# Optimization experiments

Measured on AMD Instinct MI355X. Metric: run time of the kernel, lower is better.

Reference implementation:

```python
import jax, jax.numpy as jnp
import numpy as np

N_DIS = 25000   # disease nodes: indices [0, 25000)
N_MIR = 25000   # mirna nodes:  indices [25000, 50000)
N = N_DIS + N_MIR
E = 600000
EMB = 128
HID = 128


def setup_inputs() -> dict:
    key = jax.random.key(0)
    ks = jax.random.split(key, 14)
    d_features = jax.random.normal(ks[0], (N_DIS, 383), jnp.float32)
    m_features = jax.random.normal(ks[1], (N_MIR, 495), jnp.float32)
    src = jax.random.randint(ks[2], (E,), 0, N, jnp.int32)
    dst = jax.random.randint(ks[3], (E,), 0, N, jnp.int32)
    def lin(k, fan_in, fan_out):
        lim = 1.0 / np.sqrt(fan_in)
        return jax.random.uniform(k, (fan_in, fan_out), jnp.float32, -lim, lim)
    return {
        "d_features": d_features,
        "m_features": m_features,
        "src": src,
        "dst": dst,
        "W_d": lin(ks[4], 383, EMB), "b_d": jnp.zeros((EMB,), jnp.float32),
        "W_m": lin(ks[5], 495, EMB), "b_m": jnp.zeros((EMB,), jnp.float32),
        "W_self1": lin(ks[6], EMB, HID), "W_neigh1": lin(ks[7], EMB, HID),
        "b1": jnp.zeros((HID,), jnp.float32),
        "W_self2": lin(ks[8], HID, HID), "W_neigh2": lin(ks[9], HID, HID),
        "b2": jnp.zeros((HID,), jnp.float32),
    }


def reference(d_features, m_features, src, dst,
              W_d, b_d, W_m, b_m,
              W_self1, W_neigh1, b1, W_self2, W_neigh2, b2):
    # Per-type embedding projection (torch.no_grad in original; dropout eval=identity)
    h_d = d_features @ W_d + b_d            # [N_DIS, EMB]
    h_m = m_features @ W_m + b_m            # [N_MIR, EMB]
    h = jnp.concatenate([h_d, h_m], axis=0)  # [N, EMB]

    # in-degree for mean aggregation (isolated nodes -> mean 0, like DGL fn.mean)
    deg = jax.ops.segment_sum(jnp.ones(src.shape, h.dtype), dst, num_segments=N)
    inv_deg = 1.0 / jnp.maximum(deg, 1.0)    # [N]

    def sage(x, W_self, W_neigh, b):
        # gather src feats, segment-mean into dst, then combine (DGL SAGEConv 'mean')
        agg = jax.ops.segment_sum(x[src], dst, num_segments=N) * inv_deg[:, None]
        return x @ W_self + agg @ W_neigh + b

    h = jax.nn.relu(sage(h, W_self1, W_neigh1, b1))
    h = sage(h, W_self2, W_neigh2, b2)
    return h
```

## Files before the change

### kernel.cpp

```cpp
#include <hip/hip_runtime.h>

#define N_DIS 25000
#define N_MIR 25000
#define NN    50000
#define E_NUM 600000
#define EMB   128

typedef __attribute__((ext_vector_type(8))) short short8v;
typedef __attribute__((ext_vector_type(4))) float floatx4;

__device__ __forceinline__ floatx4 mfma_bf16_16x16x32(short8v a, short8v b, floatx4 c) {
    asm("v_mfma_f32_16x16x32_bf16 %0, %1, %2, %0" : "+v"(c) : "v"(a), "v"(b));
    return c;
}

__device__ __forceinline__ float us2f(unsigned short u) {
    return __uint_as_float(((unsigned)u) << 16);
}
__device__ __forceinline__ unsigned short f2us(float f) {
    unsigned u = __float_as_uint(f);
    unsigned r = ((u >> 16) & 1u) + 0x7FFFu;
    u += r;
    return (unsigned short)(u >> 16);
}
__device__ __forceinline__ float loadf(const void* p, size_t i, bool isbf) {
    if (isbf) return us2f(((const unsigned short*)p)[i]);
    return ((const float*)p)[i];
}

__global__ __launch_bounds__(256) void gs_zero(int* counts, int* flags) {
    int i = blockIdx.x * blockDim.x + threadIdx.x;
    if (i < NN) counts[i] = 0;
    if (i < 8) flags[i] = 0;
}

__global__ __launch_bounds__(64) void gs_setflag(int* flags, int v) {
    if (threadIdx.x == 0) flags[0] = v;
}

__global__ __launch_bounds__(256) void gs_probe(const void* x, int* flags) {
    const unsigned* u = (const unsigned*)x;
    unsigned w = u[threadIdx.x];
    int e = (int)((w >> 7) & 0xFF);
    if (e >= 118 && e <= 135) atomicAdd(&flags[0], 1);
}

__global__ __launch_bounds__(256) void gs_prepw(const void* Wd, const void* Wm,
                                                const void* Ws1, const void* Wn1,
                                                const void* Ws2, const void* Wn2,
                                                const int* flags, unsigned short* wt) {
    const bool isbf = flags[0] > 128;
    const int t = threadIdx.x;
    const int w = blockIdx.x >> 2;
    const int cq = (blockIdx.x & 3) * 32;
    const void* W;
    unsigned short* oh;
    unsigned short* ol;
    int K, Kp;
    if (w == 0)      { W = Wd;  oh = wt + 0;      ol = wt + 49152;  K = 383; Kp = 384; }
    else if (w == 1) { W = Wm;  oh = wt + 98304;  ol = wt + 163840; K = 495; Kp = 512; }
    else if (w == 2) { W = Ws1; oh = wt + 229376; ol = wt + 245760; K = 128; Kp = 128; }
    else if (w == 3) { W = Wn1; oh = wt + 262144; ol = wt + 278528; K = 128; Kp = 128; }
    else if (w == 4) { W = Ws2; oh = wt + 294912; ol = wt + 311296; K = 128; Kp = 128; }
    else             { W = Wn2; oh = wt + 327680; ol = wt + 344064; K = 128; Kp = 128; }
    for (int c = cq; c < cq + 32; ++c) {
        for (int k = t; k < Kp; k += 256) {
            float x = (k < K) ? loadf(W, (size_t)k * EMB + c, isbf) : 0.f;
            unsigned short h = f2us(x);
            oh[(size_t)c * Kp + k] = h;
            ol[(size_t)c * Kp + k] = f2us(x - us2f(h));
        }
    }
}

__global__ __launch_bounds__(256) void gs_count(const int* dst, int* counts) {
    int e = blockIdx.x * blockDim.x + threadIdx.x;
    if (e < E_NUM) {
        unsigned d = (unsigned)dst[e];
        if (d < (unsigned)NN) atomicAdd(&counts[d], 1);
    }
}

__global__ __launch_bounds__(256) void gs_scan1(const int* counts, int* row_start, int* bsums) {
    __shared__ int tsum[256];
    const int t = threadIdx.x;
    const int base = blockIdx.x * 1024 + t * 4;
    int v0 = (base + 0 < NN) ? counts[base + 0] : 0;
    int v1 = (base + 1 < NN) ? counts[base + 1] : 0;
    int v2 = (base + 2 < NN) ? counts[base + 2] : 0;
    int v3 = (base + 3 < NN) ? counts[base + 3] : 0;
    int s = v0 + v1 + v2 + v3;
    tsum[t] = s;
    __syncthreads();
    for (int off = 1; off < 256; off <<= 1) {
        int xv = 0;
        if (t >= off) xv = tsum[t - off];
        __syncthreads();
        tsum[t] += xv;
        __syncthreads();
    }
    int excl = tsum[t] - s;
    if (base + 0 < NN) row_start[base + 0] = excl;
    excl += v0;
    if (base + 1 < NN) row_start[base + 1] = excl;
    excl += v1;
    if (base + 2 < NN) row_start[base + 2] = excl;
    excl += v2;
    if (base + 3 < NN) row_start[base + 3] = excl;
    if (t == 255) bsums[blockIdx.x] = tsum[255];
}

__global__ __launch_bounds__(64) void gs_scan2(int* bsums, int* row_start, int nb) {
    if (threadIdx.x == 0) {
        int run = 0;
        for (int i = 0; i < nb; ++i) {
            int v = bsums[i];
            bsums[i] = run;
            run += v;
        }
        row_start[NN] = run;
    }
}

__global__ __launch_bounds__(256) void gs_scan3(int* row_start, int* cursor, const int* bsums) {
    const int t = threadIdx.x;
    const int base = blockIdx.x * 1024 + t * 4;
    const int add = bsums[blockIdx.x];
    for (int i = 0; i < 4; ++i) {
        int idx = base + i;
        if (idx < NN) {
            int v = row_start[idx] + add;
            row_start[idx] = v;
            cursor[idx] = v;
        }
    }
}

__global__ __launch_bounds__(256) void gs_scatter(const int* src, const int* dst, int* cursor,
                                                  int* eidx) {
    int e = blockIdx.x * blockDim.x + threadIdx.x;
    if (e < E_NUM) {
        unsigned d = (unsigned)dst[e];
        unsigned sv = (unsigned)src[e];
        if (d < (unsigned)NN && sv < (unsigned)NN) {
            int p = atomicAdd(&cursor[d], 1);
            eidx[p] = (int)sv;
        }
    }
}

__global__ __launch_bounds__(256) void gs_agg(const float* __restrict__ x,
                                              const int* __restrict__ row_start,
                                              const int* __restrict__ eidx,
                                              float* __restrict__ agg) {
    const int t = threadIdx.x;
    const int row = blockIdx.x * 8 + (t >> 5);
    const int tc = (t & 31) * 4;
    if (row >= NN) return;
    const int s0 = row_start[row];
    const int s1 = row_start[row + 1];
    float a0x = 0.f, a0y = 0.f, a0z = 0.f, a0w = 0.f;
    float a1x = 0.f, a1y = 0.f, a1z = 0.f, a1w = 0.f;
    int e = s0;
    for (; e + 1 < s1; e += 2) {
        int sa = eidx[e];
        int sb = eidx[e + 1];
        float4 va = *(const float4*)&x[(size_t)sa * EMB + tc];
        float4 vb = *(const float4*)&x[(size_t)sb * EMB + tc];
        a0x += va.x; a0y += va.y; a0z += va.z; a0w += va.w;
        a1x += vb.x; a1y += vb.y; a1z += vb.z; a1w += vb.w;
    }
    if (e < s1) {
        int sa = eidx[e];
        float4 va = *(const float4*)&x[(size_t)sa * EMB + tc];
        a0x += va.x; a0y += va.y; a0z += va.z; a0w += va.w;
    }
    float inv = (s1 > s0) ? 1.f / (float)(s1 - s0) : 0.f;
    float4 o;
    o.x = (a0x + a1x) * inv;
    o.y = (a0y + a1y) * inv;
    o.z = (a0z + a1z) * inv;
    o.w = (a0w + a1w) * inv;
    *(float4*)&agg[(size_t)row * EMB + tc] = o;
}

__global__ __launch_bounds__(256, 3) void gs_mm(
    const void* __restrict__ Xa, int Ka, const unsigned short* __restrict__ WAh,
    const unsigned short* __restrict__ WAl, int KpA, const void* __restrict__ ba,
    const void* __restrict__ Xb, int Kb, const unsigned short* __restrict__ WBh,
    const unsigned short* __restrict__ WBl, int KpB, const void* __restrict__ bb,
    int splitB, int Ma, int Mb,
    const float* __restrict__ X2, const unsigned short* __restrict__ W2h,
    const unsigned short* __restrict__ W2l,
    const int* __restrict__ flags, float* __restrict__ out, int x1_dyn, int do_relu) {
    __shared__ __align__(16) unsigned char sm[49152];
    unsigned char* smXH = sm;
    unsigned char* smXL = sm + 8192;
    unsigned char* smWH = sm + 16384;
    unsigned char* smWL = sm + 32768;
    const bool isbf = flags[0] > 128;
    const int t = threadIdx.x;
    const bool sideB = (int)blockIdx.x >= splitB;
    const void* X1 = sideB ? Xb : Xa;
    const unsigned short* W1h = sideB ? WBh : WAh;
    const unsigned short* W1l = sideB ? WBl : WAl;
    const int K1 = sideB ? Kb : Ka;
    const int Kp1 = sideB ? KpB : KpA;
    const void* bias = sideB ? bb : ba;
    const int M = sideB ? Mb : Ma;
    const int r0 = (sideB ? ((int)blockIdx.x - splitB) : (int)blockIdx.x) * 64;
    float* outb = out + (sideB ? (size_t)Ma * EMB : 0);
    const bool x1bf = (x1_dyn != 0) && isbf;

    const int l = t & 63;
    const int wv = t >> 6;
    const int wr = wv >> 1, wc = wv & 1;
    const int lr = l & 15, lg = l >> 4;

    floatx4 acc[2][4];
#pragma unroll
    for (int rt = 0; rt < 2; ++rt)
#pragma unroll
        for (int ct = 0; ct < 4; ++ct) acc[rt][ct] = (floatx4){0.f, 0.f, 0.f, 0.f};

    const int nch1 = (K1 + 63) >> 6;
    const int totch = nch1 + (X2 ? 2 : 0);

    const int srX = t >> 2;
    const int skX = (t & 3) << 4;
    const int scW = t >> 1;
    const int skW = (t & 1) << 5;

    for (int ch = 0; ch < totch; ++ch) {
        const void* cX;
        const unsigned short* cWh;
        const unsigned short* cWl;
        int ck0, cK, cKp;
        bool cxbf;
        if (ch < nch1) {
            cX = X1; cWh = W1h; cWl = W1l; ck0 = ch << 6; cK = K1; cKp = Kp1; cxbf = x1bf;
        } else {
            cX = (const void*)X2; cWh = W2h; cWl = W2l;
            ck0 = (ch - nch1) << 6; cK = 128; cKp = 128; cxbf = false;
        }

        __syncthreads();
        {
            const int gr = r0 + srX;
            float xv[16];
            const bool vec = (!cxbf) && (cK == 128);
            if (vec) {
                if (gr < M) {
                    const float* p = &((const float*)cX)[(size_t)gr * 128 + ck0 + skX];
#pragma unroll
                    for (int q = 0; q < 4; ++q) {
                        float4 v = *(const float4*)(p + (q << 2));
                        xv[q * 4 + 0] = v.x; xv[q * 4 + 1] = v.y;
                        xv[q * 4 + 2] = v.z; xv[q * 4 + 3] = v.w;
                    }
                } else {
#pragma unroll
                    for (int j = 0; j < 16; ++j) xv[j] = 0.f;
                }
            } else {
#pragma unroll
                for (int j = 0; j < 16; ++j) {
                    int gk = ck0 + skX + j;
                    float v = 0.f;
                    if (gr < M && gk < cK)
                        v = cxbf ? us2f(((const unsigned short*)cX)[(size_t)gr * cK + gk])
                                 : ((const float*)cX)[(size_t)gr * cK + gk];
                    xv[j] = v;
                }
            }
            const int rowoff = srX << 7;
            const int swz = (srX & 7) << 4;
#pragma unroll
            for (int g = 0; g < 2; ++g) {
                short8v vh, vl;
#pragma unroll
                for (int e = 0; e < 8; ++e) {
                    float x = xv[(g << 3) + e];
                    unsigned short h = f2us(x);
                    vh[e] = (short)h;
                    vl[e] = (short)f2us(x - us2f(h));
                }
                const int off = rowoff + ((((skX << 1) + (g << 4))) ^ swz);
                *(short8v*)(smXH + off) = vh;
                *(short8v*)(smXL + off) = vl;
            }
        }
        {
            const unsigned short* ph = cWh + (size_t)scW * cKp + ck0 + skW;
            const unsigned short* pl = cWl + (size_t)scW * cKp + ck0 + skW;
            const int coff = scW << 7;
            const int csw = (scW & 7) << 4;
#pragma unroll
            for (int g = 0; g < 4; ++g) {
                short8v vh = *(const short8v*)(ph + (g << 3));
                short8v vl = *(const short8v*)(pl + (g << 3));
                const int off = coff + ((((skW << 1) + (g << 4))) ^ csw);
                *(short8v*)(smWH + off) = vh;
                *(short8v*)(smWL + off) = vl;
            }
        }
        __syncthreads();

        const bool skip_xl = cxbf;
        const bool skip_wl = isbf;
#pragma unroll
        for (int ks = 0; ks < 2; ++ks) {
            const int kbyte = (ks << 6) + (lg << 4);
            short8v ah[2], al[2];
#pragma unroll
            for (int rt = 0; rt < 2; ++rt) {
                const int row = wr * 32 + rt * 16 + lr;
                const int off = (row << 7) + (kbyte ^ ((row & 7) << 4));
                ah[rt] = *(const short8v*)(smXH + off);
                al[rt] = *(const short8v*)(smXL + off);
            }
#pragma unroll
            for (int ct = 0; ct < 4; ++ct) {
                const int col = wc * 64 + ct * 16 + lr;
                const int boff = (col << 7) + (kbyte ^ ((col & 7) << 4));
                short8v bh = *(const short8v*)(smWH + boff);
                short8v bl = *(const short8v*)(smWL + boff);
                acc[0][ct] = mfma_bf16_16x16x32(ah[0], bh, acc[0][ct]);
                acc[1][ct] = mfma_bf16_16x16x32(ah[1], bh, acc[1][ct]);
                if (!skip_xl) {
                    acc[0][ct] = mfma_bf16_16x16x32(al[0], bh, acc[0][ct]);
                    acc[1][ct] = mfma_bf16_16x16x32(al[1], bh, acc[1][ct]);
                }
                if (!skip_wl) {
                    acc[0][ct] = mfma_bf16_16x16x32(ah[0], bl, acc[0][ct]);
                    acc[1][ct] = mfma_bf16_16x16x32(ah[1], bl, acc[1][ct]);
                }
            }
        }
    }

#pragma unroll
    for (int ct = 0; ct < 4; ++ct) {
        const int col = wc * 64 + ct * 16 + lr;
        const float bbv = loadf(bias, col, isbf);
#pragma unroll
        for (int rt = 0; rt < 2; ++rt) {
#pragma unroll
            for (int rr = 0; rr < 4; ++rr) {
                const int row = r0 + wr * 32 + rt * 16 + (lg << 2) + rr;
                if (row < M) {
                    float v = acc[rt][ct][rr] + bbv;
                    if (do_relu) v = v > 0.f ? v : 0.f;
                    outb[(size_t)row * EMB + col] = v;
                }
            }
        }
    }
}

extern "C" __attribute__((visibility("default"))) void kernel_launch(
    void* const* d_in, const int* in_sizes, int n_in, void* d_out, int out_size, void* d_ws,
    size_t ws_size, hipStream_t stream) {
    int iDF = 0, iMF = 1, iSRC = 2, iDST = 3, iWD = 4, iBD = 5, iWM = 6, iBM = 7;
    int iWS1 = 8, iWN1 = 9, iB1 = 10, iWS2 = 11, iWN2 = 12, iB2 = 13;
    long u0 = in_sizes ? (long)in_sizes[0] : 9575000L;
    int dt = -1;
    if (u0 == 49024L || u0 == 98048L || u0 == 196096L) {
        iWD = 0; iWM = 1; iWN1 = 2; iWN2 = 3; iWS1 = 4; iWS2 = 5;
        iB1 = 6; iB2 = 7; iBD = 8; iBM = 9; iDF = 10; iDST = 11; iMF = 12; iSRC = 13;
        if (u0 == 98048L) dt = 1;
        else if (u0 == 196096L) dt = 0;
    } else {
        if (u0 == 19150000L) dt = 1;
        else if (u0 == 38300000L) dt = 0;
    }
    const void* d_features = d_in[iDF];
    const void* m_features = d_in[iMF];
    const int* src = (const int*)d_in[iSRC];
    const int* dst = (const int*)d_in[iDST];
    const void* W_d = d_in[iWD];
    const void* b_d = d_in[iBD];
    const void* W_m = d_in[iWM];
    const void* b_m = d_in[iBM];
    const void* W_self1 = d_in[iWS1];
    const void* W_neigh1 = d_in[iWN1];
    const void* b1 = d_in[iB1];
    const void* W_self2 = d_in[iWS2];
    const void* W_neigh2 = d_in[iWN2];
    const void* b2v = d_in[iB2];

    char* w = (char*)d_ws;
    int* flags = (int*)(w + 0);
    int* counts = (int*)(w + 64);
    int* row_start = (int*)(w + 200064);
    int* cursor = (int*)(w + 400128);
    int* bsums = (int*)(w + 600128);
    int* eidx = (int*)(w + 600384);
    unsigned short* wt = (unsigned short*)(w + 3000448);
    unsigned short* wt_hd = wt + 0;
    unsigned short* wt_ld = wt + 49152;
    unsigned short* wt_hm = wt + 98304;
    unsigned short* wt_lm = wt + 163840;
    unsigned short* wt_hs1 = wt + 229376;
    unsigned short* wt_ls1 = wt + 245760;
    unsigned short* wt_hn1 = wt + 262144;
    unsigned short* wt_ln1 = wt + 278528;
    unsigned short* wt_hs2 = wt + 294912;
    unsigned short* wt_ls2 = wt + 311296;
    unsigned short* wt_hn2 = wt + 327680;
    unsigned short* wt_ln2 = wt + 344064;
    float* hF = (float*)(w + 3721344);
    float* h1F = (float*)(w + 29321344);

    const int NB_SCAN = (NN + 1023) / 1024;
    const int EB = (E_NUM + 255) / 256;
    const int ZB = (NN + 255) / 256;

    hipLaunchKernelGGL(gs_zero, dim3(ZB), dim3(256), 0, stream, counts, flags);
    if (dt == 1)
        hipLaunchKernelGGL(gs_setflag, dim3(1), dim3(64), 0, stream, flags, 1000);
    else if (dt == 0)
        hipLaunchKernelGGL(gs_setflag, dim3(1), dim3(64), 0, stream, flags, 0);
    else
        hipLaunchKernelGGL(gs_probe, dim3(1), dim3(256), 0, stream, d_features, flags);

    hipLaunchKernelGGL(gs_prepw, dim3(24), dim3(256), 0, stream, W_d, W_m, W_self1, W_neigh1,
                       W_self2, W_neigh2, flags, wt);

    hipLaunchKernelGGL(gs_count, dim3(EB), dim3(256), 0, stream, dst, counts);
    hipLaunchKernelGGL(gs_scan1, dim3(NB_SCAN), dim3(256), 0, stream, counts, row_start, bsums);
    hipLaunchKernelGGL(gs_scan2, dim3(1), dim3(64), 0, stream, bsums, row_start, NB_SCAN);
    hipLaunchKernelGGL(gs_scan3, dim3(NB_SCAN), dim3(256), 0, stream, row_start, cursor, bsums);
    hipLaunchKernelGGL(gs_scatter, dim3(EB), dim3(256), 0, stream, src, dst, cursor, eidx);

    const int PBd = (N_DIS + 63) / 64;
    hipLaunchKernelGGL(gs_mm, dim3(2 * PBd), dim3(256), 0, stream,
                       d_features, 383, wt_hd, wt_ld, 384, b_d,
                       m_features, 495, wt_hm, wt_lm, 512, b_m,
                       PBd, N_DIS, N_MIR,
                       (const float*)nullptr, (const unsigned short*)nullptr,
                       (const unsigned short*)nullptr,
                       flags, hF, 1, 0);

    const int AB = NN / 8;
    const int GB = (NN + 63) / 64;

    hipLaunchKernelGGL(gs_agg, dim3(AB), dim3(256), 0, stream, hF, row_start, eidx,
                       (float*)d_out);
    hipLaunchKernelGGL(gs_mm, dim3(GB), dim3(256), 0, stream,
                       (const void*)hF, 128, wt_hs1, wt_ls1, 128, b1,
                       (const void*)nullptr, 0, (const unsigned short*)nullptr,
                       (const unsigned short*)nullptr, 0, (const void*)nullptr,
                       GB, NN, 0,
                       (const float*)d_out, wt_hn1, wt_ln1,
                       flags, h1F, 0, 1);

    hipLaunchKernelGGL(gs_agg, dim3(AB), dim3(256), 0, stream, h1F, row_start, eidx, hF);
    hipLaunchKernelGGL(gs_mm, dim3(GB), dim3(256), 0, stream,
                       (const void*)h1F, 128, wt_hs2, wt_ls2, 128, b2v,
                       (const void*)nullptr, 0, (const unsigned short*)nullptr,
                       (const unsigned short*)nullptr, 0, (const void*)nullptr,
                       GB, NN, 0,
                       (const float*)hF, wt_hn2, wt_ln2,
                       flags, (float*)d_out, 0, 0);
}
```

Before: 462.1 us.

## Prefetch next K-chunk into registers while MFMAs consume current LDS tile

Splits the GEMM main loop into descriptor, global-fetch and LDS-write steps. The global loads for chunk ch+1 are now issued into registers before the MFMA work on chunk ch, so load latency can overlap compute. Low-part loads and stores of X and W are skipped when the inputs are already bf16. The hi split now truncates instead of rounding, with the residual carrying the difference. This adds register pressure from the 16-word X buffer plus 8 short8v W buffers, which may reduce occupancy.

```diff
diff --git a/kernel.cpp b/kernel.cpp
--- a/kernel.cpp
+++ b/kernel.cpp
@@ -231,82 +231,108 @@
     const int scW = t >> 1;
     const int skW = (t & 1) << 5;
 
-    for (int ch = 0; ch < totch; ++ch) {
-        const void* cX;
-        const unsigned short* cWh;
-        const unsigned short* cWl;
-        int ck0, cK, cKp;
-        bool cxbf;
+    unsigned xr[16];
+    short8v wfh[4], wfl[4];
+
+    const void* cX;
+    const unsigned short* cWh;
+    const unsigned short* cWl;
+    int ck0, cK, cKp;
+    bool cxbf, cvec;
+    auto DESC = [&](int ch) {
         if (ch < nch1) {
             cX = X1; cWh = W1h; cWl = W1l; ck0 = ch << 6; cK = K1; cKp = Kp1; cxbf = x1bf;
         } else {
             cX = (const void*)X2; cWh = W2h; cWl = W2l;
             ck0 = (ch - nch1) << 6; cK = 128; cKp = 128; cxbf = false;
         }
-
-        __syncthreads();
-        {
-            const int gr = r0 + srX;
-            float xv[16];
-            const bool vec = (!cxbf) && (cK == 128);
-            if (vec) {
-                if (gr < M) {
-                    const float* p = &((const float*)cX)[(size_t)gr * 128 + ck0 + skX];
-#pragma unroll
-                    for (int q = 0; q < 4; ++q) {
-                        float4 v = *(const float4*)(p + (q << 2));
-                        xv[q * 4 + 0] = v.x; xv[q * 4 + 1] = v.y;
-                        xv[q * 4 + 2] = v.z; xv[q * 4 + 3] = v.w;
-                    }
-                } else {
-#pragma unroll
-                    for (int j = 0; j < 16; ++j) xv[j] = 0.f;
+        cvec = (!cxbf) && (cK == 128);
+    };
+
+    auto FETCH = [&]() {
+        const int gr = r0 + srX;
+        if (cvec) {
+            if (gr < M) {
+                const float* p = &((const float*)cX)[(size_t)gr * 128 + ck0 + skX];
+#pragma unroll
+                for (int q = 0; q < 4; ++q) {
+                    float4 v = *(const float4*)(p + (q << 2));
+                    xr[q * 4 + 0] = __float_as_uint(v.x);
+                    xr[q * 4 + 1] = __float_as_uint(v.y);
+                    xr[q * 4 + 2] = __float_as_uint(v.z);
+                    xr[q * 4 + 3] = __float_as_uint(v.w);
                 }
             } else {
 #pragma unroll
-                for (int j = 0; j < 16; ++j) {
-                    int gk = ck0 + skX + j;
-                    float v = 0.f;
-                    if (gr < M && gk < cK)
-                        v = cxbf ? us2f(((const unsigned short*)cX)[(size_t)gr * cK + gk])
-                                 : ((const float*)cX)[(size_t)gr * cK + gk];
-                    xv[j] = v;
-                }
-            }
-            const int rowoff = srX << 7;
-            const int swz = (srX & 7) << 4;
-#pragma unroll
-            for (int g = 0; g < 2; ++g) {
-                short8v vh, vl;
-#pragma unroll
-                for (int e = 0; e < 8; ++e) {
-                    float x = xv[(g << 3) + e];
-                    unsigned short h = f2us(x);
-                    vh[e] = (short)h;
-                    vl[e] = (short)f2us(x - us2f(h));
-                }
-                const int off = rowoff + ((((skX << 1) + (g << 4))) ^ swz);
-                *(short8v*)(smXH + off) = vh;
-                *(short8v*)(smXL + off) = vl;
+                for (int j = 0; j < 16; ++j) xr[j] = 0u;
+            }
+        } else {
+#pragma unroll
+            for (int j = 0; j < 16; ++j) {
+                int gk = ck0 + skX + j;
+                unsigned v = 0u;
+                if (gr < M && gk < cK)
+                    v = cxbf ? (unsigned)((const unsigned short*)cX)[(size_t)gr * cK + gk]
+                             : ((const unsigned*)cX)[(size_t)gr * cK + gk];
+                xr[j] = v;
             }
         }
         {
             const unsigned short* ph = cWh + (size_t)scW * cKp + ck0 + skW;
-            const unsigned short* pl = cWl + (size_t)scW * cKp + ck0 + skW;
-            const int coff = scW << 7;
-            const int csw = (scW & 7) << 4;
-#pragma unroll
-            for (int g = 0; g < 4; ++g) {
-                short8v vh = *(const short8v*)(ph + (g << 3));
-                short8v vl = *(const short8v*)(pl + (g << 3));
-                const int off = coff + ((((skW << 1) + (g << 4))) ^ csw);
-                *(short8v*)(smWH + off) = vh;
-                *(short8v*)(smWL + off) = vl;
-            }
-        }
+#pragma unroll
+            for (int g = 0; g < 4; ++g) wfh[g] = *(const short8v*)(ph + (g << 3));
+            if (!isbf) {
+                const unsigned short* pl = cWl + (size_t)scW * cKp + ck0 + skW;
+#pragma unroll
+                for (int g = 0; g < 4; ++g) wfl[g] = *(const short8v*)(pl + (g << 3));
+            }
+        }
+    };
+
+    auto WRITE = [&](bool xbf) {
+        const int rowoff = srX << 7;
+        const int swz = (srX & 7) << 4;
+#pragma unroll
+        for (int g = 0; g < 2; ++g) {
+            short8v vh, vl;
+#pragma unroll
+            for (int e = 0; e < 8; ++e) {
+                unsigned u = xr[(g << 3) + e];
+                if (xbf) {
+                    vh[e] = (short)u;
+                    vl[e] = 0;
+                } else {
+                    unsigned short h = (unsigned short)(u >> 16);
+                    vh[e] = (short)h;
+                    vl[e] = (short)f2us(__uint_as_float(u) - us2f(h));
+                }
+            }
+            const int off = rowoff + ((((skX << 1) + (g << 4))) ^ swz);
+            *(short8v*)(smXH + off) = vh;
+            if (!xbf) *(short8v*)(smXL + off) = vl;
+        }
+        const int coff = scW << 7;
+        const int csw = (scW & 7) << 4;
+#pragma unroll
+        for (int g = 0; g < 4; ++g) {
+            const int off = coff + ((((skW << 1) + (g << 4))) ^ csw);
+            *(short8v*)(smWH + off) = wfh[g];
+            if (!isbf) *(short8v*)(smWL + off) = wfl[g];
+        }
+    };
+
+    DESC(0);
+    FETCH();
+    for (int ch = 0; ch < totch; ++ch) {
+        const bool xbf = cxbf;
         __syncthreads();
-
-        const bool skip_xl = cxbf;
+        WRITE(xbf);
+        __syncthreads();
+        if (ch + 1 < totch) {
+            DESC(ch + 1);
+            FETCH();
+        }
+        const bool skip_xl = xbf;
         const bool skip_wl = isbf;
 #pragma unroll
         for (int ks = 0; ks < 2; ++ks) {
@@ -317,14 +343,13 @@
                 const int row = wr * 32 + rt * 16 + lr;
                 const int off = (row << 7) + (kbyte ^ ((row & 7) << 4));
                 ah[rt] = *(const short8v*)(smXH + off);
-                al[rt] = *(const short8v*)(smXL + off);
+                if (!skip_xl) al[rt] = *(const short8v*)(smXL + off);
             }
 #pragma unroll
             for (int ct = 0; ct < 4; ++ct) {
                 const int col = wc * 64 + ct * 16 + lr;
                 const int boff = (col << 7) + (kbyte ^ ((col & 7) << 4));
                 short8v bh = *(const short8v*)(smWH + boff);
-                short8v bl = *(const short8v*)(smWL + boff);
                 acc[0][ct] = mfma_bf16_16x16x32(ah[0], bh, acc[0][ct]);
                 acc[1][ct] = mfma_bf16_16x16x32(ah[1], bh, acc[1][ct]);
                 if (!skip_xl) {
@@ -332,6 +357,7 @@
                     acc[1][ct] = mfma_bf16_16x16x32(al[1], bh, acc[1][ct]);
                 }
                 if (!skip_wl) {
+                    short8v bl = *(const short8v*)(smWL + boff);
                     acc[0][ct] = mfma_bf16_16x16x32(ah[0], bl, acc[0][ct]);
                     acc[1][ct] = mfma_bf16_16x16x32(ah[1], bl, acc[1][ct]);
                 }
```

New measurement: 472.6 us. 1.02x slower.
